# Performance work log

Hardware: AMD Instinct MI355X
Metric: run time of the kernel (lower is better)

Reference implementation:

```python
import jax, jax.numpy as jnp
import numpy as np

B, H, W = 64, 512, 512
CD = 400                      # center_dims
MS_H = MS_W = 10              # max shifts
EPS = 1e-8
C_X = (H - CD) // 2           # 56
C_Y = (W - CD) // 2           # 56


def _conv_valid(x, k):
    # x: [B,h,w,1], k: [kh,kw,1,1] -> VALID conv, stride 1
    return jax.lax.conv_general_dilated(
        x, k, window_strides=(1, 1), padding='VALID',
        dimension_numbers=('NHWC', 'HWIO', 'NHWC'))


def setup_inputs() -> dict:
    key = jax.random.key(0)
    k1, k2 = jax.random.split(key)
    # smooth low-frequency template (so NCC peak neighborhood is positive -> log() finite)
    coarse = jax.random.normal(k1, (32, 32), dtype=jnp.float32)
    template = jax.image.resize(coarse, (H, W), method='bilinear')
    template = template - template.min() + 1.0  # keep positive-ish intensities
    noise = 0.05 * jax.random.normal(k2, (B, H, W, 1), dtype=jnp.float32)
    x = template[None, :, :, None] + noise
    return {'x': x, 'template': template}


def reference(x, template):
    # --- template normalization (init-time in the TF layer) ---
    tmpl = template[MS_W + C_X: H - (MS_W + C_X), MS_H + C_Y: W - (MS_H + C_Y)]  # [380,380]
    tmpl = tmpl[:, :, None, None].astype(jnp.float32)                            # HWIO
    t_zm = tmpl - jnp.mean(tmpl, axis=(0, 1), keepdims=True)
    t_var = jnp.sum(jnp.square(t_zm), axis=(0, 1), keepdims=True) + EPS          # [1,1,1,1]

    # --- image normalization ---
    Xc = x[:, C_X:H - C_X, C_Y:W - C_Y, :]                                       # [B,400,400,1]
    imgs_zm = Xc - jnp.mean(Xc, axis=(1, 2), keepdims=True)
    ones_k = jnp.ones_like(tmpl)
    localsum_sq = _conv_valid(jnp.square(Xc), ones_k)                            # [B,21,21,1]
    localsum = _conv_valid(Xc, ones_k)
    n_t = float(np.prod(tmpl.shape))
    imgs_var = localsum_sq - jnp.square(localsum) / n_t + EPS
    imgs_var = jnp.where(imgs_var < 0, jnp.zeros_like(imgs_var), imgs_var)

    # --- NCC ---
    denominator = jnp.sqrt(t_var * imgs_var)
    numerator = _conv_valid(imgs_zm, t_zm)
    ncc = numerator / denominator
    ncc = jnp.where(jnp.isnan(ncc), jnp.zeros_like(ncc), ncc)                    # [B,21,21,1]

    # --- integer argmax + gaussian (log-parabola) subpixel interpolation ---
    ncc2 = ncc[..., 0]                                                           # [B,21,21]
    ww = ncc2.shape[2]
    am = jnp.argmax(ncc2.reshape(B, -1), axis=1)
    sh_x = (am // ww).astype(jnp.int32)
    sh_y = (am % ww).astype(jnp.int32)
    log_ncc = jnp.log(ncc2)
    bidx = jnp.arange(B)

    def g(dx, dy):
        return log_ncc[bidx, sh_x + dx, sh_y + dy]

    log_xm1_y = g(-1, 0); log_xp1_y = g(1, 0)
    log_x_ym1 = g(0, -1); log_x_yp1 = g(0, 1)
    four_log_xy = 4.0 * g(0, 0)
    sh_x_n = (-(sh_x - MS_H)).astype(jnp.float32) - (log_xm1_y - log_xp1_y) / (
        2.0 * log_xm1_y - four_log_xy + 2.0 * log_xp1_y)
    sh_y_n = (-(sh_y - MS_W)).astype(jnp.float32) - (log_x_ym1 - log_x_yp1) / (
        2.0 * log_x_ym1 - four_log_xy + 2.0 * log_x_yp1)

    # --- bilinear translate: translations=[dx,dy]=[sh_y_n, sh_x_n]; out(r,c)=in(r-dy, c-dx), fill 0 ---
    def warp_one(img, dy, dx):
        rr = jnp.arange(H, dtype=jnp.float32)[:, None] - dy    # [H,1]
        cc = jnp.arange(W, dtype=jnp.float32)[None, :] - dx    # [1,W]
        r0 = jnp.floor(rr); c0 = jnp.floor(cc)
        wr = rr - r0; wc = cc - c0
        r0i = jnp.broadcast_to(r0.astype(jnp.int32), (H, W))
        c0i = jnp.broadcast_to(c0.astype(jnp.int32), (H, W))

        def samp(ri, ci):
            valid = (ri >= 0) & (ri < H) & (ci >= 0) & (ci < W)
            v = img[jnp.clip(ri, 0, H - 1), jnp.clip(ci, 0, W - 1)]
            return jnp.where(valid, v, 0.0)

        v00 = samp(r0i, c0i); v01 = samp(r0i, c0i + 1)
        v10 = samp(r0i + 1, c0i); v11 = samp(r0i + 1, c0i + 1)
        return (v00 * (1 - wr) * (1 - wc) + v01 * (1 - wr) * wc
                + v10 * wr * (1 - wc) + v11 * wr * wc)

    warped = jax.vmap(warp_one)(x[..., 0], sh_x_n, sh_y_n)     # [B,H,W]
    # transpose [0,2,1] then flatten, matching the TF layer's output layout
    return jnp.transpose(warped, (0, 2, 1)).reshape(B, H * W)
```

## Files before the change

### kernel.cpp

```cpp
#include <hip/hip_runtime.h>
#include <math.h>

#define HH 512
#define WW 512
#define NB 64
#define CXY 56
#define TOFF 66
#define TN 380
#define XN 400
#define NL 21
#define N_T 144400.0f
#define EPSF 1e-8f
#define NUT 32
#define SXS 424

#define TPART_S   0
#define TPART_S2  384
#define TSTATS    768
#define ROWSUM    1024
#define ROWSUMSQ  (ROWSUM + 537600)
#define CCPART2   1024
#define LOCALSUM  1076224
#define LOCALSQ   (LOCALSUM + 28224)
#define SHIFTS    1132672
#define SHIFTSI   (SHIFTS + 128)
#define EXACTN    (SHIFTSI + 128)
#define TSHIFT_F  (EXACTN + 384)
#define XF16      (TSHIFT_F + 1677312)

typedef _Float16 half2_t __attribute__((ext_vector_type(2)));
typedef _Float16 f16x8 __attribute__((ext_vector_type(8)));
typedef float f32x4 __attribute__((ext_vector_type(4)));

__global__ __launch_bounds__(128) void k_tstats1(const float* __restrict__ tpl,
                                                 float* __restrict__ ws) {
    int u = blockIdx.x;
    int l = threadIdx.x;
    const float* row = tpl + (TOFF + u) * WW + TOFF;
    float s = 0.f, s2 = 0.f;
    for (int v = l; v < TN; v += 128) { float t = row[v]; s += t; s2 += t * t; }
    for (int off = 32; off; off >>= 1) { s += __shfl_down(s, off); s2 += __shfl_down(s2, off); }
    __shared__ float rs[2], rs2[2];
    int wid = l >> 6;
    if ((l & 63) == 0) { rs[wid] = s; rs2[wid] = s2; }
    __syncthreads();
    if (l == 0) { ws[TPART_S + u] = rs[0] + rs[1]; ws[TPART_S2 + u] = rs2[0] + rs2[1]; }
}

__global__ __launch_bounds__(512) void k_tstats2(float* __restrict__ ws) {
    int l = threadIdx.x;
    float s  = (l < TN) ? ws[TPART_S + l]  : 0.f;
    float s2 = (l < TN) ? ws[TPART_S2 + l] : 0.f;
    for (int off = 32; off; off >>= 1) { s += __shfl_down(s, off); s2 += __shfl_down(s2, off); }
    __shared__ float rs[8], rs2[8];
    int wid = l >> 6;
    if ((l & 63) == 0) { rs[wid] = s; rs2[wid] = s2; }
    __syncthreads();
    if (l == 0) {
        float S = 0.f, S2 = 0.f;
        for (int k = 0; k < 8; ++k) { S += rs[k]; S2 += rs2[k]; }
        float mu = S / N_T;
        ws[TSTATS] = mu;
        ws[TSTATS + 1] = S2 - S * mu + EPSF;
    }
}

__global__ __launch_bounds__(256) void k_tshift(const float* __restrict__ tpl,
                                                float* __restrict__ ws) {
    int u = blockIdx.x;
    int j = blockIdx.y;
    float mu = ws[TSTATS];
    _Float16* dst = (_Float16*)(ws + TSHIFT_F) + ((size_t)j * 384 + u) * 416;
    for (int c = threadIdx.x; c < 416; c += 256) {
        float v = 0.f;
        int vs = c - j;
        if (u < TN && vs >= 0 && vs < TN) v = tpl[(TOFF + u) * WW + TOFF + vs] - mu;
        dst[c] = (_Float16)v;
    }
}

__global__ __launch_bounds__(256) void k_rowsum(const float* __restrict__ x,
                                                float* __restrict__ ws) {
    __shared__ float sm[4][416];
    int wid = threadIdx.x >> 6, lane = threadIdx.x & 63;
    int row = blockIdx.x * 4 + wid;
    int b = row / 416, p = row - b * 416;
    const float* xr = x + ((size_t)b * HH + (CXY + p)) * WW + CXY;
    _Float16* xh = (_Float16*)(ws + XF16) + ((size_t)b * 416 + p) * 416;
    float s = 0.f, s2 = 0.f;
    for (int v = lane; v < 416; v += 64) {
        float t = xr[v];
        sm[wid][v] = t;
        xh[v] = (_Float16)t;
        if (v < TN) { s += t; s2 += t * t; }
    }
    for (int off = 32; off; off >>= 1) { s += __shfl_down(s, off); s2 += __shfl_down(s2, off); }
    __syncthreads();
    if (lane == 0 && p < XN) {
        float* rs  = ws + ROWSUM   + (size_t)(b * XN + p) * NL;
        float* rq  = ws + ROWSUMSQ + (size_t)(b * XN + p) * NL;
        float w = s, w2 = s2;
        rs[0] = w; rq[0] = w2;
        for (int j = 1; j < NL; ++j) {
            float a = sm[wid][j - 1], bv = sm[wid][j + TN - 1];
            w  += bv - a;
            w2 += bv * bv - a * a;
            rs[j] = w; rq[j] = w2;
        }
    }
}

__global__ __launch_bounds__(512) void k_vert(float* __restrict__ ws) {
    int b = blockIdx.x, half = blockIdx.y, t = threadIdx.x;
    __shared__ float sm[XN * 22];
    const float* src = ws + (half ? ROWSUMSQ : ROWSUM) + (size_t)b * (XN * NL);
    for (int k = t; k < XN * NL; k += 512) {
        int p = k / NL, j = k - p * NL;
        sm[p * 22 + j] = src[k];
    }
    __syncthreads();
    if (t < NL * NL) {
        int i = t / NL, j = t - i * NL;
        const float* base = sm + i * 22 + j;
        float s0 = 0.f, s1 = 0.f, s2 = 0.f, s3 = 0.f;
        for (int p = 0; p < TN; p += 4) {
            s0 += base[p * 22];
            s1 += base[(p + 1) * 22];
            s2 += base[(p + 2) * 22];
            s3 += base[(p + 3) * 22];
        }
        ws[(half ? LOCALSQ : LOCALSUM) + b * (NL * NL) + t] = (s0 + s1) + (s2 + s3);
    }
}

__global__ __launch_bounds__(256) void k_ccm(float* __restrict__ ws) {
    const int b = blockIdx.x, ut = blockIdx.y;
    const int U = 12 * ut;
    const int tid = threadIdx.x;
    const int lane = tid & 63, wv = tid >> 6;
    __shared__ __align__(16) _Float16 sX[32 * SXS];
    __shared__ float sD[4][16][34];

    {
        const _Float16* src0 = (const _Float16*)(ws + XF16)
                             + ((size_t)b * 416 + U) * 416;
        for (int c = tid; c < 32 * 52; c += 256) {
            int r = c / 52, c8 = c - r * 52;
            *reinterpret_cast<f16x8*>(sX + r * SXS + c8 * 8) =
                *reinterpret_cast<const f16x8*>(src0 + (size_t)r * 416 + c8 * 8);
        }
    }
    __syncthreads();

    const _Float16* tsh = (const _Float16*)(ws + TSHIFT_F);
    const int r16 = lane & 15, h8 = (lane >> 4) * 8;
    const int rbase = (lane >> 4) * 4, cbase = lane & 15;
    const _Float16* bb0 = sX + r16 * SXS + h8;

    for (int gi = 0; gi < 2; ++gi) {
        const int g = wv + 4 * gi;
        if (g >= 7) break;
        const int j0 = 3 * g;
        const _Float16* a0 = tsh + ((size_t)(j0    ) * 384 + U + r16) * 416 + h8;
        const _Float16* a1 = tsh + ((size_t)(j0 + 1) * 384 + U + r16) * 416 + h8;
        const _Float16* a2 = tsh + ((size_t)(j0 + 2) * 384 + U + r16) * 416 + h8;

        f32x4 c00 = {0.f, 0.f, 0.f, 0.f};
        f32x4 c01 = c00, c10 = c00, c11 = c00, c20 = c00, c21 = c00;
        f16x8 A0 = *reinterpret_cast<const f16x8*>(a0);
        f16x8 A1 = *reinterpret_cast<const f16x8*>(a1);
        f16x8 A2 = *reinterpret_cast<const f16x8*>(a2);
#pragma unroll
        for (int kc = 0; kc < 13; ++kc) {
            f16x8 N0 = A0, N1 = A1, N2 = A2;
            if (kc < 12) {
                N0 = *reinterpret_cast<const f16x8*>(a0 + (kc + 1) * 32);
                N1 = *reinterpret_cast<const f16x8*>(a1 + (kc + 1) * 32);
                N2 = *reinterpret_cast<const f16x8*>(a2 + (kc + 1) * 32);
            }
            f16x8 B0 = *reinterpret_cast<const f16x8*>(bb0 + kc * 32);
            f16x8 B1 = *reinterpret_cast<const f16x8*>(bb0 + 16 * SXS + kc * 32);
            __builtin_amdgcn_s_setprio(1);
            c00 = __builtin_amdgcn_mfma_f32_16x16x32_f16(A0, B0, c00, 0, 0, 0);
            c01 = __builtin_amdgcn_mfma_f32_16x16x32_f16(A0, B1, c01, 0, 0, 0);
            c10 = __builtin_amdgcn_mfma_f32_16x16x32_f16(A1, B0, c10, 0, 0, 0);
            c11 = __builtin_amdgcn_mfma_f32_16x16x32_f16(A1, B1, c11, 0, 0, 0);
            c20 = __builtin_amdgcn_mfma_f32_16x16x32_f16(A2, B0, c20, 0, 0, 0);
            c21 = __builtin_amdgcn_mfma_f32_16x16x32_f16(A2, B1, c21, 0, 0, 0);
            __builtin_amdgcn_s_setprio(0);
            A0 = N0; A1 = N1; A2 = N2;
        }

#pragma unroll
        for (int jj = 0; jj < 3; ++jj) {
            f32x4 d0 = (jj == 0) ? c00 : (jj == 1) ? c10 : c20;
            f32x4 d1 = (jj == 0) ? c01 : (jj == 1) ? c11 : c21;
#pragma unroll
            for (int q = 0; q < 4; ++q) {
                sD[wv][rbase + q][cbase]      = d0[q];
                sD[wv][rbase + q][16 + cbase] = d1[q];
            }
            if (lane < NL) {
                float s = 0.f;
#pragma unroll
                for (int row = 0; row < 12; ++row) s += sD[wv][row][row + lane];
                ws[CCPART2 + ((size_t)(b * NUT + ut)) * 441 + lane * NL + (j0 + jj)] = s;
            }
        }
    }
}

__global__ __launch_bounds__(512) void k_ncc(float* __restrict__ ws) {
    int b = blockIdx.x, t = threadIdx.x;
    __shared__ float vbuf[512];
    __shared__ int   ibuf[512];
    float val = -1e30f;
    if (t < NL * NL) {
        float num = 0.f;
        for (int ut = 0; ut < NUT; ++ut)
            num += ws[CCPART2 + ((size_t)(b * NUT + ut)) * 441 + t];
        float ls  = ws[LOCALSUM + b * (NL * NL) + t];
        float lsq = ws[LOCALSQ  + b * (NL * NL) + t];
        float ivar = lsq - ls * ls * (1.0f / N_T) + EPSF;
        if (ivar < 0.f) ivar = 0.f;
        float den = sqrtf(ws[TSTATS + 1] * ivar);
        float ncc = num / den;
        if (ncc != ncc) ncc = 0.f;
        val = ncc;
    }
    vbuf[t] = val; ibuf[t] = t;
    __syncthreads();
    for (int off = 256; off; off >>= 1) {
        if (t < off) {
            float v1 = vbuf[t], v2 = vbuf[t + off];
            int   i1 = ibuf[t], i2 = ibuf[t + off];
            if (v2 > v1 || (v2 == v1 && i2 < i1)) { vbuf[t] = v2; ibuf[t] = i2; }
        }
        __syncthreads();
    }
    if (t == 0) {
        int am = ibuf[0];
        ws[SHIFTSI + 2 * b]     = (float)(am / NL);
        ws[SHIFTSI + 2 * b + 1] = (float)(am % NL);
    }
}

__global__ __launch_bounds__(512) void k_exact1(const float* __restrict__ x,
                                                const float* __restrict__ tpl,
                                                float* __restrict__ ws) {
    const int b = blockIdx.x, k = blockIdx.y;
    const int sx = (int)ws[SHIFTSI + 2 * b];
    const int sy = (int)ws[SHIFTSI + 2 * b + 1];
    const int dxs[5] = {0, -1, 1, 0, 0};
    const int dys[5] = {0, 0, 0, -1, 1};
    const int px = min(max(sx + dxs[k], 0), NL - 1);
    const int py = min(max(sy + dys[k], 0), NL - 1);
    const float mu = ws[TSTATS];
    const int lane = threadIdx.x & 63, wv = threadIdx.x >> 6;
    float a = 0.f;
    for (int t = wv; t < TN; t += 8) {
        const float* trow = tpl + (TOFF + t) * WW + TOFF;
        const float* xrow = x + ((size_t)b * HH + (CXY + px + t)) * WW + CXY + py;
#pragma unroll
        for (int it = 0; it < 6; ++it) {
            int v = lane + it * 64;
            if (v < TN) a = fmaf(trow[v] - mu, xrow[v], a);
        }
    }
    for (int off = 32; off; off >>= 1) a += __shfl_down(a, off);
    __shared__ float part[8];
    if (lane == 0) part[wv] = a;
    __syncthreads();
    if (threadIdx.x == 0) {
        float s = 0.f;
        for (int w = 0; w < 8; ++w) s += part[w];
        ws[EXACTN + b * 5 + k] = s;
    }
}

__global__ __launch_bounds__(64) void k_sub(float* __restrict__ ws) {
    int b = threadIdx.x;
    if (b >= NB) return;
    int sx = (int)ws[SHIFTSI + 2 * b];
    int sy = (int)ws[SHIFTSI + 2 * b + 1];
    int lxm = max(sx - 1, 0), lxp = min(sx + 1, NL - 1);
    int lym = max(sy - 1, 0), lyp = min(sy + 1, NL - 1);
    float tvar = ws[TSTATS + 1];
    int cells[5] = { sx * NL + sy, lxm * NL + sy, lxp * NL + sy,
                     sx * NL + lym, sx * NL + lyp };
    float l[5];
    for (int k = 0; k < 5; ++k) {
        float num = ws[EXACTN + b * 5 + k];
        float ls  = ws[LOCALSUM + b * (NL * NL) + cells[k]];
        float lsq = ws[LOCALSQ  + b * (NL * NL) + cells[k]];
        float ivar = lsq - ls * ls * (1.0f / N_T) + EPSF;
        if (ivar < 0.f) ivar = 0.f;
        float ncc = num / sqrtf(tvar * ivar);
        if (ncc != ncc) ncc = 0.f;
        l[k] = logf(ncc);
    }
    float shx = -(float)(sx - 10) - (l[1] - l[2]) / (2.f * l[1] - 4.f * l[0] + 2.f * l[2]);
    float shy = -(float)(sy - 10) - (l[3] - l[4]) / (2.f * l[3] - 4.f * l[0] + 2.f * l[4]);
    ws[SHIFTS + 2 * b]     = shx;
    ws[SHIFTS + 2 * b + 1] = shy;
}

__global__ __launch_bounds__(256) void k_warp(const float* __restrict__ x,
                                              const float* __restrict__ ws,
                                              float* __restrict__ out) {
    const int b = blockIdx.z;
    const int R = blockIdx.x * 64;
    const int C = blockIdx.y * 64;
    const float dy = ws[SHIFTS + 2 * b], dx = ws[SHIFTS + 2 * b + 1];
    const int rlo = (int)floorf((float)R - dy);
    const int clo = (int)floorf((float)C - dx);
    const float wr = ((float)R - dy) - (float)rlo;
    const float wc = ((float)C - dx) - (float)clo;
    __shared__ float sm[66][67];
    const float* img = x + (size_t)b * (HH * WW);

    for (int k = threadIdx.x; k < 66 * 66; k += 256) {
        int kr = k / 66, kc = k - kr * 66;
        int ri = min(max(rlo + kr, 0), HH - 1);
        int ci = min(max(clo + kc, 0), WW - 1);
        sm[kr][kc] = img[ri * WW + ci];
    }
    __syncthreads();

    const int dr = threadIdx.x & 63;
    const int cq = threadIdx.x >> 6;
    const int r  = R + dr;
    const int r0 = rlo + dr;
    const float w00 = (1.f - wr) * (1.f - wc), w01 = (1.f - wr) * wc;
    const float w10 = wr * (1.f - wc),         w11 = wr * wc;
    const bool vr0 = (r0 >= 0) & (r0 < HH);
    const bool vr1 = (r0 + 1 >= 0) & (r0 + 1 < HH);
#pragma unroll
    for (int ci = 0; ci < 16; ++ci) {
        int dc = cq * 16 + ci;
        int c  = C + dc;
        int c0 = clo + dc;
        bool vc0 = (c0 >= 0) & (c0 < WW);
        bool vc1 = (c0 + 1 >= 0) & (c0 + 1 < WW);
        float v00 = (vr0 & vc0) ? sm[dr][dc]         : 0.f;
        float v01 = (vr0 & vc1) ? sm[dr][dc + 1]     : 0.f;
        float v10 = (vr1 & vc0) ? sm[dr + 1][dc]     : 0.f;
        float v11 = (vr1 & vc1) ? sm[dr + 1][dc + 1] : 0.f;
        float o = v00 * w00 + v01 * w01 + v10 * w10 + v11 * w11;
        out[(size_t)b * (HH * WW) + (size_t)c * HH + r] = o;
    }
}

extern "C" void kernel_launch(void* const* d_in, const int* in_sizes, int n_in,
                              void* d_out, int out_size, void* d_ws, size_t ws_size,
                              hipStream_t stream) {
    const float* x   = (const float*)d_in[0];
    const float* tpl = (const float*)d_in[1];
    float* out = (float*)d_out;
    float* ws  = (float*)d_ws;

    k_tstats1<<<TN, 128, 0, stream>>>(tpl, ws);
    k_tstats2<<<1, 512, 0, stream>>>(ws);
    k_tshift<<<dim3(384, NL), 256, 0, stream>>>(tpl, ws);
    k_rowsum<<<(NB * 416) / 4, 256, 0, stream>>>(x, ws);
    k_vert<<<dim3(NB, 2), 512, 0, stream>>>(ws);
    k_ccm<<<dim3(NB, NUT), 256, 0, stream>>>(ws);
    k_ncc<<<NB, 512, 0, stream>>>(ws);
    k_exact1<<<dim3(NB, 5), 512, 0, stream>>>(x, tpl, ws);
    k_sub<<<1, 64, 0, stream>>>(ws);
    k_warp<<<dim3(8, 8, NB), dim3(256), 0, stream>>>(x, ws, out);
}
```

Baseline: 160.1 us.

## Fuse five-point exact NCC correlation and subpixel fit into one kernel

Replaces the per-neighbour exact correlation kernel (5 blocks per batch) and the separate subpixel kernel with one kernel per batch. Each block computes all five correlations at once, reusing each template value across five accumulators, then does the log-parabola fit in thread 0. This removes one launch and cuts template reads, but the grid shrinks from 320 blocks to 64, so fewer CUs are busy during the correlation.

```diff
diff --git a/kernel.cpp b/kernel.cpp
--- a/kernel.cpp
+++ b/kernel.cpp
@@ -245,64 +245,71 @@
     }
 }
 
-__global__ __launch_bounds__(512) void k_exact1(const float* __restrict__ x,
-                                                const float* __restrict__ tpl,
-                                                float* __restrict__ ws) {
-    const int b = blockIdx.x, k = blockIdx.y;
+__global__ __launch_bounds__(512) void k_exact(const float* __restrict__ x,
+                                               const float* __restrict__ tpl,
+                                               float* __restrict__ ws) {
+    const int b = blockIdx.x;
     const int sx = (int)ws[SHIFTSI + 2 * b];
     const int sy = (int)ws[SHIFTSI + 2 * b + 1];
-    const int dxs[5] = {0, -1, 1, 0, 0};
-    const int dys[5] = {0, 0, 0, -1, 1};
-    const int px = min(max(sx + dxs[k], 0), NL - 1);
-    const int py = min(max(sy + dys[k], 0), NL - 1);
+    const int lxm = max(sx - 1, 0), lxp = min(sx + 1, NL - 1);
+    const int lym = max(sy - 1, 0), lyp = min(sy + 1, NL - 1);
     const float mu = ws[TSTATS];
     const int lane = threadIdx.x & 63, wv = threadIdx.x >> 6;
-    float a = 0.f;
+    float a0 = 0.f, a1 = 0.f, a2 = 0.f, a3 = 0.f, a4 = 0.f;
     for (int t = wv; t < TN; t += 8) {
         const float* trow = tpl + (TOFF + t) * WW + TOFF;
-        const float* xrow = x + ((size_t)b * HH + (CXY + px + t)) * WW + CXY + py;
+        const float* r0 = x + ((size_t)b * HH + (CXY + sx  + t)) * WW + CXY;
+        const float* r1 = x + ((size_t)b * HH + (CXY + lxm + t)) * WW + CXY;
+        const float* r2 = x + ((size_t)b * HH + (CXY + lxp + t)) * WW + CXY;
 #pragma unroll
         for (int it = 0; it < 6; ++it) {
             int v = lane + it * 64;
-            if (v < TN) a = fmaf(trow[v] - mu, xrow[v], a);
-        }
-    }
-    for (int off = 32; off; off >>= 1) a += __shfl_down(a, off);
-    __shared__ float part[8];
-    if (lane == 0) part[wv] = a;
+            if (v < TN) {
+                float tz = trow[v] - mu;
+                a0 = fmaf(tz, r0[sy  + v], a0);
+                a1 = fmaf(tz, r1[sy  + v], a1);
+                a2 = fmaf(tz, r2[sy  + v], a2);
+                a3 = fmaf(tz, r0[lym + v], a3);
+                a4 = fmaf(tz, r0[lyp + v], a4);
+            }
+        }
+    }
+    for (int off = 32; off; off >>= 1) {
+        a0 += __shfl_down(a0, off); a1 += __shfl_down(a1, off);
+        a2 += __shfl_down(a2, off); a3 += __shfl_down(a3, off);
+        a4 += __shfl_down(a4, off);
+    }
+    __shared__ float red[8][5];
+    if (lane == 0) {
+        red[wv][0] = a0; red[wv][1] = a1; red[wv][2] = a2;
+        red[wv][3] = a3; red[wv][4] = a4;
+    }
     __syncthreads();
     if (threadIdx.x == 0) {
-        float s = 0.f;
-        for (int w = 0; w < 8; ++w) s += part[w];
-        ws[EXACTN + b * 5 + k] = s;
-    }
-}
-
-__global__ __launch_bounds__(64) void k_sub(float* __restrict__ ws) {
-    int b = threadIdx.x;
-    if (b >= NB) return;
-    int sx = (int)ws[SHIFTSI + 2 * b];
-    int sy = (int)ws[SHIFTSI + 2 * b + 1];
-    int lxm = max(sx - 1, 0), lxp = min(sx + 1, NL - 1);
-    int lym = max(sy - 1, 0), lyp = min(sy + 1, NL - 1);
-    float tvar = ws[TSTATS + 1];
-    int cells[5] = { sx * NL + sy, lxm * NL + sy, lxp * NL + sy,
-                     sx * NL + lym, sx * NL + lyp };
-    float l[5];
-    for (int k = 0; k < 5; ++k) {
-        float num = ws[EXACTN + b * 5 + k];
-        float ls  = ws[LOCALSUM + b * (NL * NL) + cells[k]];
-        float lsq = ws[LOCALSQ  + b * (NL * NL) + cells[k]];
-        float ivar = lsq - ls * ls * (1.0f / N_T) + EPSF;
-        if (ivar < 0.f) ivar = 0.f;
-        float ncc = num / sqrtf(tvar * ivar);
-        if (ncc != ncc) ncc = 0.f;
-        l[k] = logf(ncc);
-    }
-    float shx = -(float)(sx - 10) - (l[1] - l[2]) / (2.f * l[1] - 4.f * l[0] + 2.f * l[2]);
-    float shy = -(float)(sy - 10) - (l[3] - l[4]) / (2.f * l[3] - 4.f * l[0] + 2.f * l[4]);
-    ws[SHIFTS + 2 * b]     = shx;
-    ws[SHIFTS + 2 * b + 1] = shy;
+        float n[5];
+        for (int k = 0; k < 5; ++k) {
+            float s = 0.f;
+            for (int w = 0; w < 8; ++w) s += red[w][k];
+            n[k] = s;
+        }
+        const float tvar = ws[TSTATS + 1];
+        const int cells[5] = { sx * NL + sy, lxm * NL + sy, lxp * NL + sy,
+                               sx * NL + lym, sx * NL + lyp };
+        float l[5];
+        for (int k = 0; k < 5; ++k) {
+            float ls  = ws[LOCALSUM + b * (NL * NL) + cells[k]];
+            float lsq = ws[LOCALSQ  + b * (NL * NL) + cells[k]];
+            float ivar = lsq - ls * ls * (1.0f / N_T) + EPSF;
+            if (ivar < 0.f) ivar = 0.f;
+            float ncc = n[k] / sqrtf(tvar * ivar);
+            if (ncc != ncc) ncc = 0.f;
+            l[k] = logf(ncc);
+        }
+        float shx = -(float)(sx - 10) - (l[1] - l[2]) / (2.f * l[1] - 4.f * l[0] + 2.f * l[2]);
+        float shy = -(float)(sy - 10) - (l[3] - l[4]) / (2.f * l[3] - 4.f * l[0] + 2.f * l[4]);
+        ws[SHIFTS + 2 * b]     = shx;
+        ws[SHIFTS + 2 * b + 1] = shy;
+    }
 }
 
 __global__ __launch_bounds__(256) void k_warp(const float* __restrict__ x,
@@ -366,7 +373,6 @@
     k_vert<<<dim3(NB, 2), 512, 0, stream>>>(ws);
     k_ccm<<<dim3(NB, NUT), 256, 0, stream>>>(ws);
     k_ncc<<<NB, 512, 0, stream>>>(ws);
-    k_exact1<<<dim3(NB, 5), 512, 0, stream>>>(x, tpl, ws);
-    k_sub<<<1, 64, 0, stream>>>(ws);
+    k_exact<<<NB, 512, 0, stream>>>(x, tpl, ws);
     k_warp<<<dim3(8, 8, NB), dim3(256), 0, stream>>>(x, ws, out);
 }
```

Result: slower. 168.2 us (+5.1%).
